# Performance work log

Measured on AMD Instinct MI355X. Metric: run time of the kernel, lower is better.

Reference implementation:

```python
import jax, jax.numpy as jnp
import numpy as np

VISION_TOKEN_TYPE = 1

def _swiglu_mlp(x, w_gate, w_up, w_down):
    # x: [B, L, D]; w_gate/w_up: [D, F]; w_down: [F, D]
    g = jax.nn.silu(jnp.einsum('bld,df->blf', x, w_gate))
    u = jnp.einsum('bld,df->blf', x, w_up)
    return jnp.einsum('blf,fd->bld', g * u, w_down)

def _vision_mask(token_type_ids):
    # vision_token_mask[:, :-1] = (tt[:, :-1]==V) & (tt[:, 1:]==V); last col False
    is_v = token_type_ids == VISION_TOKEN_TYPE
    pair = is_v[:, :-1] & is_v[:, 1:]
    return jnp.concatenate([pair, jnp.zeros_like(pair[:, :1])], axis=1)  # [B, L] bool

def setup_inputs() -> dict:
    key = jax.random.key(0)
    ks = jax.random.split(key, 8)
    B, L, D, F = 2, 2048, 4096, 11008
    s = 0.02
    return {
        'hidden_states': jax.random.normal(ks[0], (B, L, D), dtype=jnp.float32),
        'token_type_ids': jax.random.randint(ks[1], (B, L), 0, 2, dtype=jnp.int64),
        'vision_gate': jax.random.normal(ks[2], (D, F), dtype=jnp.float32) * s,
        'vision_up': jax.random.normal(ks[3], (D, F), dtype=jnp.float32) * s,
        'vision_down': jax.random.normal(ks[4], (F, D), dtype=jnp.float32) * s,
        'language_gate': jax.random.normal(ks[5], (D, F), dtype=jnp.float32) * s,
        'language_up': jax.random.normal(ks[6], (D, F), dtype=jnp.float32) * s,
        'language_down': jax.random.normal(ks[7], (F, D), dtype=jnp.float32) * s,
    }

def reference(hidden_states, token_type_ids, vision_gate, vision_up, vision_down,
              language_gate, language_up, language_down):
    vmask = _vision_mask(token_type_ids)  # [B, L]
    out_v = _swiglu_mlp(hidden_states, vision_gate, vision_up, vision_down)
    out_l = _swiglu_mlp(hidden_states, language_gate, language_up, language_down)
    return jnp.where(vmask[:, :, None], out_v, out_l)
```

## Files before the change

kernel.cpp:

```cpp
#include <hip/hip_runtime.h>
#include <hip/hip_bf16.h>

#define B_    2
#define L_    2048
#define D_    4096
#define F_    11008
#define M_TOK (B_ * L_)
#define BM    256
#define M_ALLOC (M_TOK + BM)
#define NTM   (M_ALLOC / BM)
#define NT_GU (D_ / 64)
#define NT_DN (F_ / 64)
#define NTILE_F (F_ / 128)
#define SPLITK_DN 4
#define LDS_GU 131072
#define LDS_DN 131072

typedef __attribute__((ext_vector_type(8))) __bf16 bf16x8;
typedef __attribute__((ext_vector_type(4))) float  f32x4;
typedef unsigned short ushort_t;
typedef unsigned int   uint_t;


__device__ __forceinline__ void gload_lds16(const void* g, void* l) {
  __builtin_amdgcn_global_load_lds(
      (const __attribute__((address_space(1))) void*)g,
      (__attribute__((address_space(3))) void*)l, 16, 0, 0);
}

#define SCHED0()  __builtin_amdgcn_sched_barrier(0)
#define PH_BAR()  { __builtin_amdgcn_sched_barrier(0); __builtin_amdgcn_s_barrier(); __builtin_amdgcn_sched_barrier(0); }
#define LGKM(n)   { asm volatile("s_waitcnt lgkmcnt(" #n ")" ::: "memory"); __builtin_amdgcn_sched_barrier(0); }
#define VM4()     { asm volatile("s_waitcnt vmcnt(4)" ::: "memory"); __builtin_amdgcn_sched_barrier(0); }
#define VM0()     { asm volatile("s_waitcnt vmcnt(0)" ::: "memory"); __builtin_amdgcn_sched_barrier(0); }
#define PRIO1()   __builtin_amdgcn_s_setprio(1)
#define PRIO0()   __builtin_amdgcn_s_setprio(0)

__device__ __forceinline__ ushort_t f2bf(float v) {
  union { __hip_bfloat16 h; ushort_t u; } cv;
  cv.h = __float2bfloat16(v);
  return cv.u;
}

__device__ __forceinline__ int xcd_swz(int orig, int nwg) {
  const int q = nwg >> 3, r = nwg & 7, xcd = orig & 7;
  return (xcd < r ? xcd * (q + 1) : r * (q + 1) + (xcd - r) * q) + (orig >> 3);
}

__device__ __forceinline__ void stage_half(const __hip_bfloat16* __restrict__ src, int ldE,
                                           __bf16* ldsb, int w, int lane) {
#pragma unroll
  for (int j = 0; j < 2; ++j) {
    const int ch  = (w * 2 + j) * 64 + lane;
    const int row = ch >> 3;
    const int cc  = (ch & 7) ^ (row & 7);
    gload_lds16(src + (size_t)(row * ldE + cc * 8), ldsb + (w * 2 + j) * 512);
  }
}

__device__ __forceinline__ bf16x8 ldfrag(const __bf16* region, int row, int koffb) {
  const int off = ((row << 7) + koffb) ^ ((row & 7) << 4);
  return *(const bf16x8*)((const char*)region + off);
}

__device__ __forceinline__ void mfma_q(f32x4 (&acc)[8][4], int mb, int nb,
                                       const bf16x8 (&af)[4][2], const bf16x8 (&bf)[2][2]) {
#pragma unroll
  for (int mm = 0; mm < 4; ++mm)
#pragma unroll
    for (int nn = 0; nn < 2; ++nn)
#pragma unroll
      for (int ks = 0; ks < 2; ++ks)
        acc[mb + mm][nb + nn] = __builtin_amdgcn_mfma_f32_16x16x32_bf16(
            af[mm][ks], bf[nn][ks], acc[mb + mm][nb + nn], 0, 0, 0);
}

__device__ __forceinline__ void gemm_kloop(const __hip_bfloat16* __restrict__ Ag, const int ldA,
                                           const __hip_bfloat16* __restrict__ Bg, const int ldB,
                                           const int nt, __bf16* smem, f32x4 (&acc)[8][4],
                                           const int wm, const int wn, const int l15,
                                           const int l4, const int w, const int lane) {
  stage_half(Ag,             ldA, smem,          w, lane);
  stage_half(Ag + 128 * ldA, ldA, smem + 8192,   w, lane);
  stage_half(Bg,             ldB, smem + 32768,  w, lane);
  stage_half(Bg + 128 * ldB, ldB, smem + 40960,  w, lane);
  if (1 < nt) {
    stage_half(Ag + 64,             ldA, smem + 16384, w, lane);
    stage_half(Ag + 64 + 128 * ldA, ldA, smem + 24576, w, lane);
  }
  VM4(); PH_BAR();

  for (int t = 0; t < nt; ++t) {
    const int cur = t & 1;
    const __bf16* At = smem + cur * 16384;
    const __bf16* Bt = smem + 32768 + cur * 16384;
    __bf16* nxA = smem + cur * 16384;
    __bf16* nxB = smem + 32768 + (cur ^ 1) * 16384;
    bf16x8 a0[4][2], a1[4][2], b0[2][2], b1[2][2];

#pragma unroll
    for (int i = 0; i < 4; ++i)
#pragma unroll
      for (int ks = 0; ks < 2; ++ks)
        a0[i][ks] = ldfrag(At, wm * 128 + i * 16 + l15, ks * 64 + l4 * 16);
#pragma unroll
    for (int n = 0; n < 2; ++n)
#pragma unroll
      for (int ks = 0; ks < 2; ++ks)
        b0[n][ks] = ldfrag(Bt, wn * 64 + n * 16 + l15, ks * 64 + l4 * 16);
    SCHED0();
#pragma unroll
    for (int i = 0; i < 4; ++i)
#pragma unroll
      for (int ks = 0; ks < 2; ++ks)
        a1[i][ks] = ldfrag(At, wm * 128 + 64 + i * 16 + l15, ks * 64 + l4 * 16);
    SCHED0();
#pragma unroll
    for (int n = 0; n < 2; ++n)
#pragma unroll
      for (int ks = 0; ks < 2; ++ks)
        b1[n][ks] = ldfrag(Bt, wn * 64 + 32 + n * 16 + l15, ks * 64 + l4 * 16);
    SCHED0();
    if (t + 1 < nt) {
      stage_half(Bg + (t + 1) * 64,             ldB, nxB,        w, lane);
      stage_half(Bg + (t + 1) * 64 + 128 * ldB, ldB, nxB + 8192, w, lane);
    }
    SCHED0();
    LGKM(12);
    PRIO1(); mfma_q(acc, 0, 0, a0, b0); PRIO0();
    LGKM(4);
    PRIO1(); mfma_q(acc, 4, 0, a1, b0); PRIO0();
    LGKM(0);
    PH_BAR();
    if (t + 2 < nt) {
      stage_half(Ag + (t + 2) * 64,             ldA, nxA,        w, lane);
      stage_half(Ag + (t + 2) * 64 + 128 * ldA, ldA, nxA + 8192, w, lane);
    }
    SCHED0();
    PRIO1();
    mfma_q(acc, 4, 2, a1, b1);
    mfma_q(acc, 0, 2, a0, b1);
    PRIO0();
    if (t + 2 < nt) { VM4(); } else { VM0(); }
    PH_BAR();
  }
}


__global__ void init_kernel(int* counters, int* slot2tok) {
  int i = blockIdx.x * 256 + threadIdx.x;
  if (i < 2) counters[i] = 0;
  if (i < M_ALLOC) slot2tok[i] = -1;
}

__global__ void assign_kernel(const int* __restrict__ tt, int* counters,
                              int* __restrict__ slot2tok) {
  int t = blockIdx.x * 256 + threadIdx.x;
  if (t >= M_TOK) return;
  int l = t & (L_ - 1);
  bool isv = (tt[t] == 1) && (l < L_ - 1) && (tt[t + 1] == 1);
  int slot;
  if (isv) slot = atomicAdd(&counters[0], 1);
  else     slot = M_ALLOC - 1 - atomicAdd(&counters[1], 1);
  slot2tok[slot] = t;
}

__global__ void gather_cvt(const float* __restrict__ x, const int* __restrict__ slot2tok,
                           __hip_bfloat16* __restrict__ xg) {
  const int s = blockIdx.x;
  const int t = slot2tok[s];
  __hip_bfloat16* dst = xg + (size_t)s * D_ + threadIdx.x * 16;
  union { ushort_t h[8]; uint4 v; } p0, p1;
  if (t >= 0) {
    const float4* s4 = (const float4*)(x + (size_t)t * D_ + threadIdx.x * 16);
    float4 a = s4[0], b = s4[1], c = s4[2], d = s4[3];
    float vals[16] = {a.x,a.y,a.z,a.w,b.x,b.y,b.z,b.w,c.x,c.y,c.z,c.w,d.x,d.y,d.z,d.w};
#pragma unroll
    for (int i = 0; i < 8; ++i) p0.h[i] = f2bf(vals[i]);
#pragma unroll
    for (int i = 0; i < 8; ++i) p1.h[i] = f2bf(vals[8 + i]);
  } else {
    p0.v = make_uint4(0, 0, 0, 0);
    p1.v = make_uint4(0, 0, 0, 0);
  }
  *(uint4*)dst = p0.v;
  *(uint4*)(dst + 8) = p1.v;
}

__global__ __launch_bounds__(256) void transpose_cvt_lds6(
    const float* __restrict__ s0, const float* __restrict__ s1,
    const float* __restrict__ s2, const float* __restrict__ s3,
    const float* __restrict__ s4, const float* __restrict__ s5,
    __hip_bfloat16* __restrict__ d0, __hip_bfloat16* __restrict__ d1,
    __hip_bfloat16* __restrict__ d2, __hip_bfloat16* __restrict__ d3,
    __hip_bfloat16* __restrict__ d4, __hip_bfloat16* __restrict__ d5) {
  const float* in;
  __hip_bfloat16* out;
  switch (blockIdx.y) {
    case 0:  in = s0; out = d0; break;
    case 1:  in = s1; out = d1; break;
    case 2:  in = s2; out = d2; break;
    case 3:  in = s3; out = d3; break;
    case 4:  in = s4; out = d4; break;
    default: in = s5; out = d5; break;
  }
  const int R = (blockIdx.y < 4) ? D_ : F_;
  const int C = (blockIdx.y < 4) ? F_ : D_;
  __shared__ float tile[64][65];
  const int cb = C >> 6;
  const int c0 = (blockIdx.x % cb) * 64;
  const int r0 = (blockIdx.x / cb) * 64;
  const int tx = threadIdx.x & 63;
  const int ty = threadIdx.x >> 6;
#pragma unroll
  for (int j = 0; j < 16; ++j) {
    const int r = ty + 4 * j;
    tile[r][tx] = in[(size_t)(r0 + r) * C + c0 + tx];
  }
  __syncthreads();
  const int rr2 = (threadIdx.x & 31) * 2;
  const int cc  = threadIdx.x >> 5;
#pragma unroll
  for (int j = 0; j < 8; ++j) {
    const int c = cc + 8 * j;
    const uint_t lo = f2bf(tile[rr2][c]);
    const uint_t hi = f2bf(tile[rr2 + 1][c]);
    *(uint_t*)(out + (size_t)(c0 + c) * R + r0 + rr2) = lo | (hi << 16);
  }
}

__global__ void sentinel_kernel(float* out, int n) {
  int i = blockIdx.x * 256 + threadIdx.x;
  if (i < n) out[i] = 1e30f;
}

__global__ __launch_bounds__(512, 2) void gemm256_gateup_fused(
    const __hip_bfloat16* __restrict__ Xg,
    const __hip_bfloat16* __restrict__ WgTv, const __hip_bfloat16* __restrict__ WuTv,
    const __hip_bfloat16* __restrict__ WgTl, const __hip_bfloat16* __restrict__ WuTl,
    __hip_bfloat16* __restrict__ H, const int* __restrict__ counters) {
  extern __shared__ __bf16 smem[];
  const int tid = threadIdx.x, lane = tid & 63, w = tid >> 6;
  const int wm = w >> 1, wn = w & 1;
  const int l15 = lane & 15, l4 = lane >> 4;

  const int wg = xcd_swz(blockIdx.x, gridDim.x);
  const int mt = wg % NTM, ntile = wg / NTM;
  const int row0 = mt * BM;
  const int ncol0 = ntile * 128;
  const int nv = counters[0];
  const bool isv = row0 < nv;
  const __hip_bfloat16* Ag   = Xg + (size_t)row0 * D_;
  const __hip_bfloat16* Bg_g = (isv ? WgTv : WgTl) + (size_t)ncol0 * D_;
  const __hip_bfloat16* Bu_g = (isv ? WuTv : WuTl) + (size_t)ncol0 * D_;

  f32x4 accg[4][4] = {};
  f32x4 accu[4][4] = {};
  const int nt = NT_GU;

  stage_half(Ag,                  D_, smem,          w, lane);
  stage_half(Ag + 128 * D_,       D_, smem + 8192,   w, lane);
  stage_half(Bg_g,                D_, smem + 32768,  w, lane);
  stage_half(Bu_g,                D_, smem + 49152,  w, lane);
  stage_half(Ag + 64,             D_, smem + 16384,  w, lane);
  stage_half(Ag + 64 + 128 * D_,  D_, smem + 24576,  w, lane);
  VM4(); PH_BAR();

  for (int t = 0; t < nt; ++t) {
    const int cur = t & 1;
    const __bf16* At  = smem + cur * 16384;
    const __bf16* Bgt = smem + 32768 + cur * 8192;
    const __bf16* But = smem + 49152 + cur * 8192;
    __bf16* nxA  = smem + cur * 16384;
    __bf16* nxBg = smem + 32768 + (cur ^ 1) * 8192;
    __bf16* nxBu = smem + 49152 + (cur ^ 1) * 8192;
    bf16x8 af[4][2], bg[4][2], bu[4][2];

#pragma unroll
    for (int m = 0; m < 2; ++m)
#pragma unroll
      for (int ks = 0; ks < 2; ++ks)
        af[m][ks] = ldfrag(At, wm * 64 + m * 16 + l15, ks * 64 + l4 * 16);
#pragma unroll
    for (int n = 0; n < 4; ++n)
#pragma unroll
      for (int ks = 0; ks < 2; ++ks)
        bg[n][ks] = ldfrag(Bgt, wn * 64 + n * 16 + l15, ks * 64 + l4 * 16);
    SCHED0();
#pragma unroll
    for (int m = 2; m < 4; ++m)
#pragma unroll
      for (int ks = 0; ks < 2; ++ks)
        af[m][ks] = ldfrag(At, wm * 64 + m * 16 + l15, ks * 64 + l4 * 16);
    SCHED0();
#pragma unroll
    for (int n = 0; n < 4; ++n)
#pragma unroll
      for (int ks = 0; ks < 2; ++ks)
        bu[n][ks] = ldfrag(But, wn * 64 + n * 16 + l15, ks * 64 + l4 * 16);
    SCHED0();
    if (t + 1 < nt) {
      stage_half(Bg_g + (t + 1) * 64, D_, nxBg, w, lane);
      stage_half(Bu_g + (t + 1) * 64, D_, nxBu, w, lane);
    }
    SCHED0();
    LGKM(12);
    PRIO1();
#pragma unroll
    for (int m = 0; m < 2; ++m)
#pragma unroll
      for (int n = 0; n < 4; ++n)
#pragma unroll
        for (int ks = 0; ks < 2; ++ks)
          accg[m][n] = __builtin_amdgcn_mfma_f32_16x16x32_bf16(
              af[m][ks], bg[n][ks], accg[m][n], 0, 0, 0);
    PRIO0();
    LGKM(8);
    PRIO1();
#pragma unroll
    for (int m = 2; m < 4; ++m)
#pragma unroll
      for (int n = 0; n < 4; ++n)
#pragma unroll
        for (int ks = 0; ks < 2; ++ks)
          accg[m][n] = __builtin_amdgcn_mfma_f32_16x16x32_bf16(
              af[m][ks], bg[n][ks], accg[m][n], 0, 0, 0);
    PRIO0();
    LGKM(0);
    PH_BAR();
    if (t + 2 < nt) {
      stage_half(Ag + (t + 2) * 64,            D_, nxA,        w, lane);
      stage_half(Ag + (t + 2) * 64 + 128 * D_, D_, nxA + 8192, w, lane);
    }
    SCHED0();
    PRIO1();
#pragma unroll
    for (int m = 0; m < 4; ++m)
#pragma unroll
      for (int n = 0; n < 4; ++n)
#pragma unroll
        for (int ks = 0; ks < 2; ++ks)
          accu[m][n] = __builtin_amdgcn_mfma_f32_16x16x32_bf16(
              af[m][ks], bu[n][ks], accu[m][n], 0, 0, 0);
    PRIO0();
    if (t + 2 < nt) { VM4(); } else { VM0(); }
    PH_BAR();
  }

#pragma unroll
  for (int m = 0; m < 4; ++m) {
    const int grow = row0 + wm * 64 + m * 16 + l4 * 4;
#pragma unroll
    for (int rr = 0; rr < 4; ++rr) {
      __hip_bfloat16* orow = H + (size_t)(grow + rr) * F_ + ncol0 + wn * 64 + l15;
#pragma unroll
      for (int n = 0; n < 4; ++n) {
        const float g = accg[m][n][rr];
        const float u = accu[m][n][rr];
        orow[n * 16] = __float2bfloat16(g / (1.0f + __expf(-g)) * u);
      }
    }
  }
}


__global__ __launch_bounds__(512, 2) void gemm256_down(
    const __hip_bfloat16* __restrict__ H,
    const __hip_bfloat16* __restrict__ WdTv, const __hip_bfloat16* __restrict__ WdTl,
    float* __restrict__ out, const int* __restrict__ counters,
    const int* __restrict__ slot2tok) {
  extern __shared__ __bf16 smem[];
  const int tid = threadIdx.x, lane = tid & 63, w = tid >> 6;
  const int wm = w >> 2, wn = w & 3;
  const int l15 = lane & 15, l4 = lane >> 4;

  const int wg = xcd_swz(blockIdx.x, gridDim.x);
  const int mt = wg % NTM, ntt = wg / NTM;
  const int z  = blockIdx.y;
  const int row0 = mt * BM;
  const int ncol0 = ntt * 256;
  const int ntz = NT_DN / SPLITK_DN;
  const int t0 = z * ntz;
  const int nv = counters[0];
  const __hip_bfloat16* Bsrc = (row0 < nv) ? WdTv : WdTl;
  const __hip_bfloat16* Ag = H + (size_t)row0 * F_ + t0 * 64;
  const __hip_bfloat16* Bg = Bsrc + (size_t)ncol0 * F_ + t0 * 64;

  f32x4 acc[8][4] = {};
  gemm_kloop(Ag, F_, Bg, F_, ntz, smem, acc, wm, wn, l15, l4, w, lane);

#pragma unroll
  for (int m = 0; m < 8; ++m) {
    const int slot = row0 + wm * 128 + m * 16 + l4 * 4;
#pragma unroll
    for (int rr = 0; rr < 4; ++rr) {
      const int tok = slot2tok[slot + rr];
      if (tok < 0) continue;
      float* orow = out + (size_t)tok * D_ + ncol0 + wn * 64 + l15;
#pragma unroll
      for (int n = 0; n < 4; ++n)
        atomicAdd(&orow[n * 16], acc[m][n][rr]);
    }
  }
}


extern "C" void kernel_launch(void* const* d_in, const int* in_sizes, int n_in,
                              void* d_out, int out_size, void* d_ws, size_t ws_size,
                              hipStream_t stream) {
  const float* x   = (const float*)d_in[0];
  const int*   tt  = (const int*)d_in[1];
  const float* wgv = (const float*)d_in[2];
  const float* wuv = (const float*)d_in[3];
  const float* wdv = (const float*)d_in[4];
  const float* wgl = (const float*)d_in[5];
  const float* wul = (const float*)d_in[6];
  const float* wdl = (const float*)d_in[7];
  float* out = (float*)d_out;

  size_t off = 0;
  auto nalign = [](size_t v) { return (v + 255) & ~(size_t)255; };
  const size_t o_cnt = off; off += nalign(2 * sizeof(int));
  const size_t o_s2t = off; off += nalign((size_t)M_ALLOC * sizeof(int));
  const size_t o_xg  = off; off += nalign((size_t)M_ALLOC * D_ * 2);
  const size_t o_h   = off; off += nalign((size_t)M_ALLOC * F_ * 2);
  const size_t wbytes = nalign((size_t)D_ * F_ * 2);
  const size_t o_wgv = off; off += wbytes;
  const size_t o_wuv = off; off += wbytes;
  const size_t o_wgl = off; off += wbytes;
  const size_t o_wul = off; off += wbytes;
  const size_t o_wdv = off; off += wbytes;
  const size_t o_wdl = off; off += wbytes;

  if (ws_size < off) {
    sentinel_kernel<<<(out_size + 255) / 256, 256, 0, stream>>>(out, out_size);
    return;
  }

  char* ws = (char*)d_ws;
  int* counters = (int*)(ws + o_cnt);
  int* slot2tok = (int*)(ws + o_s2t);
  __hip_bfloat16* Xg  = (__hip_bfloat16*)(ws + o_xg);
  __hip_bfloat16* H   = (__hip_bfloat16*)(ws + o_h);
  __hip_bfloat16* WgTv = (__hip_bfloat16*)(ws + o_wgv);
  __hip_bfloat16* WuTv = (__hip_bfloat16*)(ws + o_wuv);
  __hip_bfloat16* WgTl = (__hip_bfloat16*)(ws + o_wgl);
  __hip_bfloat16* WuTl = (__hip_bfloat16*)(ws + o_wul);
  __hip_bfloat16* WdTv = (__hip_bfloat16*)(ws + o_wdv);
  __hip_bfloat16* WdTl = (__hip_bfloat16*)(ws + o_wdl);

  hipFuncSetAttribute((const void*)gemm256_gateup_fused,
                      hipFuncAttributeMaxDynamicSharedMemorySize, LDS_GU);
  hipFuncSetAttribute((const void*)gemm256_down,
                      hipFuncAttributeMaxDynamicSharedMemorySize, LDS_DN);

  hipMemsetAsync(out, 0, (size_t)out_size * sizeof(float), stream);

  init_kernel<<<(M_ALLOC + 255) / 256, 256, 0, stream>>>(counters, slot2tok);
  assign_kernel<<<(M_TOK + 255) / 256, 256, 0, stream>>>(tt, counters, slot2tok);
  gather_cvt<<<M_ALLOC, 256, 0, stream>>>(x, slot2tok, Xg);

  const int tblocks = (F_ / 64) * (D_ / 64);
  transpose_cvt_lds6<<<dim3(tblocks, 6), 256, 0, stream>>>(
      wgv, wuv, wgl, wul, wdv, wdl, WgTv, WuTv, WgTl, WuTl, WdTv, WdTl);

  gemm256_gateup_fused<<<dim3(NTM * NTILE_F), 512, LDS_GU, stream>>>(
      Xg, WgTv, WuTv, WgTl, WuTl, H, counters);

  gemm256_down<<<dim3(NTM * (D_ / 256), SPLITK_DN), 512, LDS_DN, stream>>>(
      H, WdTv, WdTl, out, counters, slot2tok);
}
```

Baseline: 1.718 ms.

## Restructure GEMM k-loop into four barrier-separated phases and reuse B fragment registers

The down-projection k-loop changes its LDS layout so each stage holds A and B together in one 32K-element buffer. It then splits each iteration into four phases, each issuing one global-to-LDS stage, a barrier, a full LDS wait and one MFMA quadrant. The gate/up kernel reuses a single B-fragment register array, loading the up fragments only after the gate MFMAs, which lowers register pressure and may raise occupancy. The cost is more barriers and full lgkm waits, which serialise LDS loads against MFMAs and reduce overlap.

```diff
diff --git a/kernel.cpp b/kernel.cpp
--- a/kernel.cpp
+++ b/kernel.cpp
@@ -80,22 +80,21 @@
                                            const int nt, __bf16* smem, f32x4 (&acc)[8][4],
                                            const int wm, const int wn, const int l15,
                                            const int l4, const int w, const int lane) {
-  stage_half(Ag,             ldA, smem,          w, lane);
-  stage_half(Ag + 128 * ldA, ldA, smem + 8192,   w, lane);
-  stage_half(Bg,             ldB, smem + 32768,  w, lane);
-  stage_half(Bg + 128 * ldB, ldB, smem + 40960,  w, lane);
+  stage_half(Ag,             ldA, smem,                w, lane);
+  stage_half(Ag + 128 * ldA, ldA, smem + 8192,         w, lane);
+  stage_half(Bg,             ldB, smem + 16384,        w, lane);
+  stage_half(Bg + 128 * ldB, ldB, smem + 24576,        w, lane);
   if (1 < nt) {
-    stage_half(Ag + 64,             ldA, smem + 16384, w, lane);
-    stage_half(Ag + 64 + 128 * ldA, ldA, smem + 24576, w, lane);
+    stage_half(Ag + 64,             ldA, smem + 32768,        w, lane);
+    stage_half(Ag + 64 + 128 * ldA, ldA, smem + 32768 + 8192, w, lane);
   }
   VM4(); PH_BAR();
 
   for (int t = 0; t < nt; ++t) {
-    const int cur = t & 1;
-    const __bf16* At = smem + cur * 16384;
-    const __bf16* Bt = smem + 32768 + cur * 16384;
-    __bf16* nxA = smem + cur * 16384;
-    __bf16* nxB = smem + 32768 + (cur ^ 1) * 16384;
+    __bf16* bufc = smem + (t & 1) * 32768;
+    __bf16* bufn = smem + ((t + 1) & 1) * 32768;
+    const __bf16* At = bufc;
+    const __bf16* Bt = bufc + 16384;
     bf16x8 a0[4][2], a1[4][2], b0[2][2], b1[2][2];
 
 #pragma unroll
@@ -108,39 +107,33 @@
 #pragma unroll
       for (int ks = 0; ks < 2; ++ks)
         b0[n][ks] = ldfrag(Bt, wn * 64 + n * 16 + l15, ks * 64 + l4 * 16);
-    SCHED0();
+    if (t + 1 < nt) stage_half(Bg + (t + 1) * 64, ldB, bufn + 16384, w, lane);
+    PH_BAR(); LGKM(0);
+    PRIO1(); mfma_q(acc, 0, 0, a0, b0); PRIO0();
+    PH_BAR();
+
 #pragma unroll
     for (int i = 0; i < 4; ++i)
 #pragma unroll
       for (int ks = 0; ks < 2; ++ks)
         a1[i][ks] = ldfrag(At, wm * 128 + 64 + i * 16 + l15, ks * 64 + l4 * 16);
-    SCHED0();
+    if (t + 1 < nt) stage_half(Bg + (t + 1) * 64 + 128 * ldB, ldB, bufn + 24576, w, lane);
+    PH_BAR(); LGKM(0);
+    PRIO1(); mfma_q(acc, 4, 0, a1, b0); PRIO0();
+    PH_BAR();
+
 #pragma unroll
     for (int n = 0; n < 2; ++n)
 #pragma unroll
       for (int ks = 0; ks < 2; ++ks)
         b1[n][ks] = ldfrag(Bt, wn * 64 + 32 + n * 16 + l15, ks * 64 + l4 * 16);
-    SCHED0();
-    if (t + 1 < nt) {
-      stage_half(Bg + (t + 1) * 64,             ldB, nxB,        w, lane);
-      stage_half(Bg + (t + 1) * 64 + 128 * ldB, ldB, nxB + 8192, w, lane);
-    }
-    SCHED0();
-    LGKM(12);
-    PRIO1(); mfma_q(acc, 0, 0, a0, b0); PRIO0();
-    LGKM(4);
-    PRIO1(); mfma_q(acc, 4, 0, a1, b0); PRIO0();
-    LGKM(0);
-    PH_BAR();
-    if (t + 2 < nt) {
-      stage_half(Ag + (t + 2) * 64,             ldA, nxA,        w, lane);
-      stage_half(Ag + (t + 2) * 64 + 128 * ldA, ldA, nxA + 8192, w, lane);
-    }
-    SCHED0();
-    PRIO1();
-    mfma_q(acc, 4, 2, a1, b1);
-    mfma_q(acc, 0, 2, a0, b1);
-    PRIO0();
+    if (t + 2 < nt) stage_half(Ag + (t + 2) * 64, ldA, bufc, w, lane);
+    PH_BAR(); LGKM(0);
+    PRIO1(); mfma_q(acc, 4, 2, a1, b1); PRIO0();
+    PH_BAR();
+
+    if (t + 2 < nt) stage_half(Ag + (t + 2) * 64 + 128 * ldA, ldA, bufc + 8192, w, lane);
+    PRIO1(); mfma_q(acc, 0, 2, a0, b1); PRIO0();
     if (t + 2 < nt) { VM4(); } else { VM0(); }
     PH_BAR();
   }
@@ -274,7 +267,7 @@
     __bf16* nxA  = smem + cur * 16384;
     __bf16* nxBg = smem + 32768 + (cur ^ 1) * 8192;
     __bf16* nxBu = smem + 49152 + (cur ^ 1) * 8192;
-    bf16x8 af[4][2], bg[4][2], bu[4][2];
+    bf16x8 af[4][2], bb[4][2];
 
 #pragma unroll
     for (int m = 0; m < 2; ++m)
@@ -285,26 +278,20 @@
     for (int n = 0; n < 4; ++n)
 #pragma unroll
       for (int ks = 0; ks < 2; ++ks)
-        bg[n][ks] = ldfrag(Bgt, wn * 64 + n * 16 + l15, ks * 64 + l4 * 16);
+        bb[n][ks] = ldfrag(Bgt, wn * 64 + n * 16 + l15, ks * 64 + l4 * 16);
     SCHED0();
 #pragma unroll
     for (int m = 2; m < 4; ++m)
 #pragma unroll
       for (int ks = 0; ks < 2; ++ks)
         af[m][ks] = ldfrag(At, wm * 64 + m * 16 + l15, ks * 64 + l4 * 16);
-    SCHED0();
-#pragma unroll
-    for (int n = 0; n < 4; ++n)
-#pragma unroll
-      for (int ks = 0; ks < 2; ++ks)
-        bu[n][ks] = ldfrag(But, wn * 64 + n * 16 + l15, ks * 64 + l4 * 16);
     SCHED0();
     if (t + 1 < nt) {
       stage_half(Bg_g + (t + 1) * 64, D_, nxBg, w, lane);
       stage_half(Bu_g + (t + 1) * 64, D_, nxBu, w, lane);
     }
     SCHED0();
-    LGKM(12);
+    LGKM(4);
     PRIO1();
 #pragma unroll
     for (int m = 0; m < 2; ++m)
@@ -313,9 +300,9 @@
 #pragma unroll
         for (int ks = 0; ks < 2; ++ks)
           accg[m][n] = __builtin_amdgcn_mfma_f32_16x16x32_bf16(
-              af[m][ks], bg[n][ks], accg[m][n], 0, 0, 0);
+              af[m][ks], bb[n][ks], accg[m][n], 0, 0, 0);
     PRIO0();
-    LGKM(8);
+    LGKM(0);
     PRIO1();
 #pragma unroll
     for (int m = 2; m < 4; ++m)
@@ -324,15 +311,21 @@
 #pragma unroll
         for (int ks = 0; ks < 2; ++ks)
           accg[m][n] = __builtin_amdgcn_mfma_f32_16x16x32_bf16(
-              af[m][ks], bg[n][ks], accg[m][n], 0, 0, 0);
+              af[m][ks], bb[n][ks], accg[m][n], 0, 0, 0);
     PRIO0();
-    LGKM(0);
+#pragma unroll
+    for (int n = 0; n < 4; ++n)
+#pragma unroll
+      for (int ks = 0; ks < 2; ++ks)
+        bb[n][ks] = ldfrag(But, wn * 64 + n * 16 + l15, ks * 64 + l4 * 16);
+    SCHED0();
     PH_BAR();
     if (t + 2 < nt) {
       stage_half(Ag + (t + 2) * 64,            D_, nxA,        w, lane);
       stage_half(Ag + (t + 2) * 64 + 128 * D_, D_, nxA + 8192, w, lane);
     }
     SCHED0();
+    LGKM(0);
     PRIO1();
 #pragma unroll
     for (int m = 0; m < 4; ++m)
@@ -341,7 +334,7 @@
 #pragma unroll
         for (int ks = 0; ks < 2; ++ks)
           accu[m][n] = __builtin_amdgcn_mfma_f32_16x16x32_bf16(
-              af[m][ks], bu[n][ks], accu[m][n], 0, 0, 0);
+              af[m][ks], bb[n][ks], accu[m][n], 0, 0, 0);
     PRIO0();
     if (t + 2 < nt) { VM4(); } else { VM0(); }
     PH_BAR();
```

Measured after the change: 1.480 ms. -13.9%, faster.
